# Optimization experiments

Hardware: AMD Instinct MI355X
Metric: run time of the kernel (lower is better)

Reference implementation:

```python
import jax, jax.numpy as jnp
import numpy as np

B, H, L, E = 32, 8, 512, 3
N_VARS = 8
TOP_P = 0.5
NOISE_EPS = 0.01
EPS = 1e-10


def setup_inputs() -> dict:
    key = jax.random.key(0)
    k1, k2, k3 = jax.random.split(key, 3)
    scale = 1.0 / np.sqrt(L)  # sane logits for softmax
    x = jax.random.normal(k1, (B, H, L, L), dtype=jnp.float32)
    gate_w = jax.random.normal(k2, (E, L), dtype=jnp.float32) * scale
    noise_w = jax.random.normal(k3, (E, L), dtype=jnp.float32) * scale
    return {"x": x, "gate_w": gate_w, "noise_w": noise_w}


def _build_masks(L, n_vars):
    # Vectorized version of the torch per-k loop building [L, 3, L] masks.
    N = L // n_vars
    j = jnp.arange(L)          # target position
    k = jnp.arange(L)[:, None]  # source position
    S = ((j % N == k % N) & (j != k)).astype(jnp.float32)   # same offset, different var
    T = ((j // N) == (k // N)).astype(jnp.float32)           # same variable block
    ST = 1.0 - S - T
    return jnp.stack([S, T, ST], axis=1)  # [L, 3, L]


def _noisy_top_p_gating(xf, gate_w, noise_w, key):
    # xf: [BH, L, L] -> logits [BH, L, E]
    clean_logits = jnp.einsum('ble,ne->bln', xf, gate_w)
    noise_stddev = jax.nn.softplus(jnp.einsum('ble,ne->bln', xf, noise_w)) + NOISE_EPS
    noisy_logits = clean_logits + jax.random.normal(key, clean_logits.shape, clean_logits.dtype) * noise_stddev
    probs = jax.nn.softmax(noisy_logits, axis=-1)  # softmax over experts (dim 2)
    # dynamic (entropy) loss: sum over L dim (dim=1), mean over rest
    loss_dynamic = -(probs * jnp.log(probs + EPS)).sum(axis=1).mean()
    # sort descending over experts
    order = jnp.argsort(-probs, axis=-1)
    sorted_probs = jnp.take_along_axis(probs, order, axis=-1)
    cum = jnp.cumsum(sorted_probs, axis=-1)
    mask = cum > TOP_P
    # keep the first expert that crosses the threshold
    thr_idx = jnp.argmax(mask.astype(jnp.int32), axis=-1)          # [BH, L]
    thr_mask = jnp.arange(E) == thr_idx[..., None]                 # one-hot bool
    mask = mask & ~thr_mask
    # scatter kept (mask==0) sorted positions back to original expert ids:
    # top_p_mask[..., sorted_indices[..., k]] = (mask[..., k] == 0)
    inv = jnp.argsort(order, axis=-1)
    top_p_mask = jnp.take_along_axis((~mask).astype(jnp.float32), inv, axis=-1)
    # importance loss on masked sorted probs summed over batch dim
    kept = jnp.where(mask, 0.0, sorted_probs)
    importance = kept.sum(axis=0)  # [L, E]
    loss_importance = jnp.var(importance, ddof=1) / (importance.mean() ** 2 + EPS)
    loss = loss_importance + 0.1 * loss_dynamic
    return top_p_mask, loss


def reference(x, gate_w, noise_w):
    Bx, Hx, Lx, _ = x.shape
    xf = x.reshape(Bx * Hx, Lx, Lx)
    gates, loss = _noisy_top_p_gating(xf, gate_w, noise_w, jax.random.key(42))
    gates = gates.reshape(Bx, Hx, Lx, E).astype(jnp.float32)
    masks = _build_masks(Lx, N_VARS)            # [L, 3, L]
    mask_base = jnp.eye(Lx, dtype=jnp.float32)[None, None]
    out = jnp.einsum('bhli,lid->bhld', gates, masks) + mask_base
    return (out, loss)
```

## Files before the change

### kernel.cpp

```cpp
#include <hip/hip_runtime.h>
#include <cstdint>
#include <cstddef>


namespace {

constexpr int kBH = 256;
constexpr int kL = 512;
constexpr int kE = 3;
constexpr int kRows = kBH * kL;

__device__ __forceinline__ uint32_t rotl32(uint32_t v, int n) {
  return (v << n) | (v >> (32 - n));
}

__device__ __forceinline__ void threefry2x32_k42(uint32_t& x0, uint32_t& x1) {
  const uint32_t ks0 = 0u;
  const uint32_t ks1 = 42u;
  const uint32_t ks2 = 0u ^ 42u ^ 0x1BD11BDAu;
  x0 += ks0; x1 += ks1;
#define TF_ROUND(r) { x0 += x1; x1 = rotl32(x1, (r)); x1 ^= x0; }
  TF_ROUND(13) TF_ROUND(15) TF_ROUND(26) TF_ROUND(6)
  x0 += ks1; x1 += ks2 + 1u;
  TF_ROUND(17) TF_ROUND(29) TF_ROUND(16) TF_ROUND(24)
  x0 += ks2; x1 += ks0 + 2u;
  TF_ROUND(13) TF_ROUND(15) TF_ROUND(26) TF_ROUND(6)
  x0 += ks0; x1 += ks1 + 3u;
  TF_ROUND(17) TF_ROUND(29) TF_ROUND(16) TF_ROUND(24)
  x0 += ks1; x1 += ks2 + 4u;
  TF_ROUND(13) TF_ROUND(15) TF_ROUND(26) TF_ROUND(6)
  x0 += ks2; x1 += ks0 + 5u;
#undef TF_ROUND
}

__device__ __forceinline__ uint32_t jax_random_bits(uint32_t flat_idx) {
  uint32_t x0 = 0u;
  uint32_t x1 = flat_idx;
  threefry2x32_k42(x0, x1);
  return x0 ^ x1;
}

__device__ float bits_to_normal(uint32_t bits) {
#pragma clang fp contract(off)
  const uint32_t fb = (bits >> 9) | 0x3F800000u;
  const float f = __uint_as_float(fb) - 1.0f;
  const float lo = -0.99999994f;
  float u = f * 2.0f + lo;
  u = fmaxf(lo, u);
  float w = -log1pf(-(u * u));
  float p;
  if (w < 5.0f) {
    w = w - 2.5f;
    p = 2.81022636e-08f;
    p = 3.43273939e-07f + p * w;
    p = -3.5233877e-06f + p * w;
    p = -4.39150654e-06f + p * w;
    p = 0.00021858087f + p * w;
    p = -0.00125372503f + p * w;
    p = -0.00417768164f + p * w;
    p = 0.246640727f + p * w;
    p = 1.50140941f + p * w;
  } else {
    w = sqrtf(w) - 3.0f;
    p = -0.000200214257f;
    p = 0.000100950558f + p * w;
    p = 0.00134934322f + p * w;
    p = -0.00367342844f + p * w;
    p = 0.00573950773f + p * w;
    p = -0.0076224613f + p * w;
    p = 0.00943887047f + p * w;
    p = 1.00167406f + p * w;
    p = 2.83297682f + p * w;
  }
  const float einv = p * u;
  return 1.41421354f * einv;
}

__device__ __forceinline__ float softplus_f32(float v) {
#pragma clang fp contract(off)
  const float amax = fmaxf(v, 0.0f);
  return amax + log1pf(expf(-fabsf(v)));
}

#define LOADG(BUF, OFF)                                                     \
  _Pragma("unroll")                                                         \
  for (int i_ = 0; i_ < 4; ++i_)                                            \
    BUF[i_] = *reinterpret_cast<const float4*>(xr + (OFF) + i_ * 4);

#define COMP16(BUF, KB)                                                     \
  {                                                                         \
    _Pragma("unroll")                                                       \
    for (int j_ = 0; j_ < 4; ++j_) {                                        \
      const int k_ = (KB) + j_ * 4;                                         \
      const float4 wg0 = *reinterpret_cast<const float4*>(gw + k_);         \
      const float4 wg1 = *reinterpret_cast<const float4*>(gw + kL + k_);    \
      const float4 wg2 = *reinterpret_cast<const float4*>(gw + 2*kL + k_);  \
      const float4 wn0 = *reinterpret_cast<const float4*>(nw + k_);         \
      const float4 wn1 = *reinterpret_cast<const float4*>(nw + kL + k_);    \
      const float4 wn2 = *reinterpret_cast<const float4*>(nw + 2*kL + k_);  \
      const float4 xq = BUF[j_];                                            \
      accg[0] = fmaf(xq.x, wg0.x, accg[0]);                                 \
      accg[1] = fmaf(xq.x, wg1.x, accg[1]);                                 \
      accg[2] = fmaf(xq.x, wg2.x, accg[2]);                                 \
      accn[0] = fmaf(xq.x, wn0.x, accn[0]);                                 \
      accn[1] = fmaf(xq.x, wn1.x, accn[1]);                                 \
      accn[2] = fmaf(xq.x, wn2.x, accn[2]);                                 \
      accg[0] = fmaf(xq.y, wg0.y, accg[0]);                                 \
      accg[1] = fmaf(xq.y, wg1.y, accg[1]);                                 \
      accg[2] = fmaf(xq.y, wg2.y, accg[2]);                                 \
      accn[0] = fmaf(xq.y, wn0.y, accn[0]);                                 \
      accn[1] = fmaf(xq.y, wn1.y, accn[1]);                                 \
      accn[2] = fmaf(xq.y, wn2.y, accn[2]);                                 \
      accg[0] = fmaf(xq.z, wg0.z, accg[0]);                                 \
      accg[1] = fmaf(xq.z, wg1.z, accg[1]);                                 \
      accg[2] = fmaf(xq.z, wg2.z, accg[2]);                                 \
      accn[0] = fmaf(xq.z, wn0.z, accn[0]);                                 \
      accn[1] = fmaf(xq.z, wn1.z, accn[1]);                                 \
      accn[2] = fmaf(xq.z, wn2.z, accn[2]);                                 \
      accg[0] = fmaf(xq.w, wg0.w, accg[0]);                                 \
      accg[1] = fmaf(xq.w, wg1.w, accg[1]);                                 \
      accg[2] = fmaf(xq.w, wg2.w, accg[2]);                                 \
      accn[0] = fmaf(xq.w, wn0.w, accn[0]);                                 \
      accn[1] = fmaf(xq.w, wn1.w, accn[1]);                                 \
      accn[2] = fmaf(xq.w, wn2.w, accn[2]);                                 \
    }                                                                       \
  }

__global__ __launch_bounds__(256) void gating_kernel(
    const float* __restrict__ x, const float* __restrict__ gw,
    const float* __restrict__ nw, float* __restrict__ g_out,
    float* __restrict__ kept_out, float* __restrict__ ent_out) {
  const int t = threadIdx.x;
  const int r = blockIdx.x * 256 + t;
  const float* xr = x + (size_t)r * kL;

  float accg[3] = {0.f, 0.f, 0.f};
  float accn[3] = {0.f, 0.f, 0.f};
  {
    float4 bufA[4], bufB[4];
    LOADG(bufA, 0)
    for (int k0 = 0; k0 < kL; k0 += 32) {
      LOADG(bufB, k0 + 16)
      COMP16(bufA, k0)
      if (k0 + 32 < kL) { LOADG(bufA, k0 + 32) }
      COMP16(bufB, k0 + 16)
    }
  }

  {
#pragma clang fp contract(off)
    float noisy[3];
    const uint32_t nbase = (uint32_t)r * 3u;
#pragma unroll
    for (int e = 0; e < 3; ++e) {
      const float cl = accg[e];
      const float sp = softplus_f32(accn[e]) + 0.01f;
      const float nz = bits_to_normal(jax_random_bits(nbase + (uint32_t)e));
      const float prod = nz * sp;
      noisy[e] = cl + prod;
    }
    const float m = fmaxf(noisy[0], fmaxf(noisy[1], noisy[2]));
    float uu[3];
    uu[0] = expf(noisy[0] - m);
    uu[1] = expf(noisy[1] - m);
    uu[2] = expf(noisy[2] - m);
    const float ssum = (uu[0] + uu[1]) + uu[2];
    float p[3];
    p[0] = uu[0] / ssum;
    p[1] = uu[1] / ssum;
    p[2] = uu[2] / ssum;

    int o0 = 0;
    if (p[1] > p[o0]) o0 = 1;
    if (p[2] > p[o0]) o0 = 2;
    const int i = (o0 == 0) ? 1 : 0;
    const int j = (o0 == 2) ? 1 : 2;
    const int o1 = (p[j] > p[i]) ? j : i;

    const float s0 = p[o0];
    const float s1 = p[o1];
    const bool keep2 = !(s0 > 0.5f);

    float g[3] = {0.f, 0.f, 0.f};
    g[o0] = 1.f;
    if (keep2) g[o1] = 1.f;

    float ent = 0.f;
    ent += p[0] * logf(p[0] + 1e-10f);
    ent += p[1] * logf(p[1] + 1e-10f);
    ent += p[2] * logf(p[2] + 1e-10f);

    const int bh = r >> 9;
    const int l = r & (kL - 1);
    g_out[r * 3 + 0] = g[0];
    g_out[r * 3 + 1] = g[1];
    g_out[r * 3 + 2] = g[2];
    kept_out[(0 * kL + l) * kBH + bh] = s0;
    kept_out[(1 * kL + l) * kBH + bh] = keep2 ? s1 : 0.f;
    kept_out[(2 * kL + l) * kBH + bh] = 0.f;
    ent_out[r] = -ent;
  }
}

__global__ __launch_bounds__(256) void loss_partial_kernel(
    const float* __restrict__ kept, const float* __restrict__ ent,
    double* __restrict__ imp_ws, double* __restrict__ ent_ws) {
  __shared__ double red[256];
  const int t = threadIdx.x;
  const int ln = t & 63;
  const int wg = blockIdx.x * 4 + (t >> 6);

#pragma unroll
  for (int rep = 0; rep < 3; ++rep) {
    const int q = wg + rep * 512;
    const float4 v = reinterpret_cast<const float4*>(kept + (size_t)q * kBH)[ln];
    double s = ((double)v.x + (double)v.y) + ((double)v.z + (double)v.w);
#pragma unroll
    for (int off = 32; off > 0; off >>= 1) s += __shfl_xor(s, off, 64);
    if (ln == 0) imp_ws[q] = s;
  }

  double a = 0.0;
#pragma unroll
  for (int it = 0; it < 4; ++it) {
    a += (double)ent[blockIdx.x * 1024 + it * 256 + t];
  }
  red[t] = a;
  __syncthreads();
  for (int off = 128; off > 0; off >>= 1) {
    if (t < off) red[t] += red[t + off];
    __syncthreads();
  }
  if (t == 0) ent_ws[blockIdx.x] = red[0];
}

__global__ __launch_bounds__(256) void loss_final_kernel(
    const double* __restrict__ imp_ws, const double* __restrict__ ent_ws,
    float* __restrict__ loss_out) {
  __shared__ double red[256];
  __shared__ double s_mean;
  const int t = threadIdx.x;

  double a = 0.0;
  for (int i = t; i < kL * kE; i += 256) a += imp_ws[i];
  red[t] = a;
  __syncthreads();
  for (int off = 128; off > 0; off >>= 1) {
    if (t < off) red[t] += red[t + off];
    __syncthreads();
  }
  if (t == 0) s_mean = red[0] / (double)(kL * kE);
  __syncthreads();
  const double mean = s_mean;

  double sq = 0.0;
  for (int i = t; i < kL * kE; i += 256) {
    const double d = imp_ws[i] - mean;
    sq += d * d;
  }
  red[t] = sq;
  __syncthreads();
  for (int off = 128; off > 0; off >>= 1) {
    if (t < off) red[t] += red[t + off];
    __syncthreads();
  }
  const double var_sum = red[0];
  __syncthreads();

  double e = 0.0;
  for (int i = t; i < 128; i += 256) e += ent_ws[i];
  red[t] = e;
  __syncthreads();
  for (int off = 128; off > 0; off >>= 1) {
    if (t < off) red[t] += red[t + off];
    __syncthreads();
  }
  if (t == 0) {
    const double var = var_sum / (double)(kL * kE - 1);
    const double loss_imp = var / (mean * mean + 1e-10);
    const double loss_dyn = red[0] / 768.0;
    loss_out[0] = (float)(loss_imp + 0.1 * loss_dyn);
  }
}

__global__ __launch_bounds__(256) void out_kernel(
    const float* __restrict__ g, float* __restrict__ out) {
  const int td = threadIdx.x;
  const int r = blockIdx.x * 8 + (td >> 5);
  const int l = r & (kL - 1);
  const float g0 = g[r * 3 + 0];
  const float g1 = g[r * 3 + 1];
  const float g2 = g[r * 3 + 2];
  const int lblk = l >> 6;
  const int loff = l & 63;
  float* orow = out + (size_t)r * kL;
  const int c0 = (td & 31) * 4;
#pragma unroll
  for (int j = 0; j < 4; ++j) {
    const int d0 = c0 + j * 128;
    float vals[4];
#pragma unroll
    for (int k = 0; k < 4; ++k) {
      const int d = d0 + k;
      float v;
      if (((d & 63) == loff) && (d != l)) v = g0;
      else if ((d >> 6) == lblk) v = g1;
      else v = g2;
      if (d == l) v += 1.0f;
      vals[k] = v;
    }
    *reinterpret_cast<float4*>(orow + d0) = *reinterpret_cast<float4*>(vals);
  }
}

}

extern "C" void kernel_launch(void* const* d_in, const int* in_sizes, int n_in,
                              void* d_out, int out_size, void* d_ws, size_t ws_size,
                              hipStream_t stream) {
  (void)in_sizes; (void)n_in; (void)out_size; (void)ws_size;
  const float* x = (const float*)d_in[0];
  const float* gw = (const float*)d_in[1];
  const float* nw = (const float*)d_in[2];
  float* out = (float*)d_out;

  float* ws = (float*)d_ws;
  float* ws_g = ws;
  float* ws_kept = ws + (size_t)kRows * 3;
  float* ws_ent = ws + (size_t)kRows * 6;
  double* ws_imp = (double*)(ws + (size_t)kRows * 7);
  double* ws_entp = ws_imp + kL * kE;

  gating_kernel<<<kRows / 256, 256, 0, stream>>>(x, gw, nw, ws_g, ws_kept, ws_ent);
  loss_partial_kernel<<<128, 256, 0, stream>>>(ws_kept, ws_ent, ws_imp, ws_entp);
  loss_final_kernel<<<1, 256, 0, stream>>>(ws_imp, ws_entp,
                                           out + (size_t)kBH * kL * kL);
  out_kernel<<<kRows / 8, 256, 0, stream>>>(ws_g, out);
}
```

Before: 142.2 us.

## Split gating dot products across six threads per row with separate epilogue kernel

The fused gating kernel gave each thread a full row and six dot products. It is now split into two kernels. A dot kernel assigns six threads to each row, one per weight vector, and writes the six accumulators to workspace. A new epilogue kernel reads them back and does the noise, softmax and top-p logic. This raises thread-level parallelism and shortens each thread's dependency chain, at the cost of an extra launch, an extra workspace round trip, and each row of x being read by six threads. Those reads hit the same cache lines but are uncoalesced across the row.

```diff
diff --git a/kernel.cpp b/kernel.cpp
--- a/kernel.cpp
+++ b/kernel.cpp
@@ -82,70 +82,54 @@
   return amax + log1pf(expf(-fabsf(v)));
 }
 
-#define LOADG(BUF, OFF)                                                     \
+#define LD4(B, P, OFF)                                                      \
   _Pragma("unroll")                                                         \
   for (int i_ = 0; i_ < 4; ++i_)                                            \
-    BUF[i_] = *reinterpret_cast<const float4*>(xr + (OFF) + i_ * 4);
-
-#define COMP16(BUF, KB)                                                     \
+    B[i_] = *reinterpret_cast<const float4*>((P) + (OFF) + i_ * 4);
+
+#define CH16(XB, WB)                                                        \
   {                                                                         \
     _Pragma("unroll")                                                       \
     for (int j_ = 0; j_ < 4; ++j_) {                                        \
-      const int k_ = (KB) + j_ * 4;                                         \
-      const float4 wg0 = *reinterpret_cast<const float4*>(gw + k_);         \
-      const float4 wg1 = *reinterpret_cast<const float4*>(gw + kL + k_);    \
-      const float4 wg2 = *reinterpret_cast<const float4*>(gw + 2*kL + k_);  \
-      const float4 wn0 = *reinterpret_cast<const float4*>(nw + k_);         \
-      const float4 wn1 = *reinterpret_cast<const float4*>(nw + kL + k_);    \
-      const float4 wn2 = *reinterpret_cast<const float4*>(nw + 2*kL + k_);  \
-      const float4 xq = BUF[j_];                                            \
-      accg[0] = fmaf(xq.x, wg0.x, accg[0]);                                 \
-      accg[1] = fmaf(xq.x, wg1.x, accg[1]);                                 \
-      accg[2] = fmaf(xq.x, wg2.x, accg[2]);                                 \
-      accn[0] = fmaf(xq.x, wn0.x, accn[0]);                                 \
-      accn[1] = fmaf(xq.x, wn1.x, accn[1]);                                 \
-      accn[2] = fmaf(xq.x, wn2.x, accn[2]);                                 \
-      accg[0] = fmaf(xq.y, wg0.y, accg[0]);                                 \
-      accg[1] = fmaf(xq.y, wg1.y, accg[1]);                                 \
-      accg[2] = fmaf(xq.y, wg2.y, accg[2]);                                 \
-      accn[0] = fmaf(xq.y, wn0.y, accn[0]);                                 \
-      accn[1] = fmaf(xq.y, wn1.y, accn[1]);                                 \
-      accn[2] = fmaf(xq.y, wn2.y, accn[2]);                                 \
-      accg[0] = fmaf(xq.z, wg0.z, accg[0]);                                 \
-      accg[1] = fmaf(xq.z, wg1.z, accg[1]);                                 \
-      accg[2] = fmaf(xq.z, wg2.z, accg[2]);                                 \
-      accn[0] = fmaf(xq.z, wn0.z, accn[0]);                                 \
-      accn[1] = fmaf(xq.z, wn1.z, accn[1]);                                 \
-      accn[2] = fmaf(xq.z, wn2.z, accn[2]);                                 \
-      accg[0] = fmaf(xq.w, wg0.w, accg[0]);                                 \
-      accg[1] = fmaf(xq.w, wg1.w, accg[1]);                                 \
-      accg[2] = fmaf(xq.w, wg2.w, accg[2]);                                 \
-      accn[0] = fmaf(xq.w, wn0.w, accn[0]);                                 \
-      accn[1] = fmaf(xq.w, wn1.w, accn[1]);                                 \
-      accn[2] = fmaf(xq.w, wn2.w, accn[2]);                                 \
+      acc = fmaf(XB[j_].x, WB[j_].x, acc);                                  \
+      acc = fmaf(XB[j_].y, WB[j_].y, acc);                                  \
+      acc = fmaf(XB[j_].z, WB[j_].z, acc);                                  \
+      acc = fmaf(XB[j_].w, WB[j_].w, acc);                                  \
     }                                                                       \
   }
 
-__global__ __launch_bounds__(256) void gating_kernel(
+__global__ __launch_bounds__(192) void dot_kernel(
     const float* __restrict__ x, const float* __restrict__ gw,
-    const float* __restrict__ nw, float* __restrict__ g_out,
+    const float* __restrict__ nw, float* __restrict__ acc_out) {
+  const int t = threadIdx.x;
+  const int row_ib = t / 6;
+  const int chain = t - row_ib * 6;
+  const int r = blockIdx.x * 32 + row_ib;
+  const float* xr = x + (size_t)r * kL;
+  const float* wr = (chain < 3) ? (gw + chain * kL) : (nw + (chain - 3) * kL);
+
+  float acc = 0.f;
+  {
+#pragma clang fp contract(off)
+    float4 xA[4], xB[4], wA[4], wB[4];
+    LD4(xA, xr, 0) LD4(wA, wr, 0)
+    for (int k0 = 0; k0 < kL; k0 += 32) {
+      LD4(xB, xr, k0 + 16) LD4(wB, wr, k0 + 16)
+      CH16(xA, wA)
+      if (k0 + 32 < kL) { LD4(xA, xr, k0 + 32) LD4(wA, wr, k0 + 32) }
+      CH16(xB, wB)
+    }
+  }
+  acc_out[(size_t)blockIdx.x * 192 + t] = acc;
+}
+
+__global__ __launch_bounds__(256) void epilogue_kernel(
+    const float* __restrict__ acc_in, float* __restrict__ g_out,
     float* __restrict__ kept_out, float* __restrict__ ent_out) {
-  const int t = threadIdx.x;
-  const int r = blockIdx.x * 256 + t;
-  const float* xr = x + (size_t)r * kL;
-
-  float accg[3] = {0.f, 0.f, 0.f};
-  float accn[3] = {0.f, 0.f, 0.f};
-  {
-    float4 bufA[4], bufB[4];
-    LOADG(bufA, 0)
-    for (int k0 = 0; k0 < kL; k0 += 32) {
-      LOADG(bufB, k0 + 16)
-      COMP16(bufA, k0)
-      if (k0 + 32 < kL) { LOADG(bufA, k0 + 32) }
-      COMP16(bufB, k0 + 16)
-    }
-  }
+  const int r = blockIdx.x * 256 + threadIdx.x;
+  const float* a = acc_in + (size_t)r * 6;
+  float accg[3] = {a[0], a[1], a[2]};
+  float accn[3] = {a[3], a[4], a[5]};
 
   {
 #pragma clang fp contract(off)
@@ -328,10 +312,12 @@
   float* ws_g = ws;
   float* ws_kept = ws + (size_t)kRows * 3;
   float* ws_ent = ws + (size_t)kRows * 6;
-  double* ws_imp = (double*)(ws + (size_t)kRows * 7);
+  float* ws_acc = ws + (size_t)kRows * 7;
+  double* ws_imp = (double*)(ws + (size_t)kRows * 13 + (size_t)kRows);
   double* ws_entp = ws_imp + kL * kE;
 
-  gating_kernel<<<kRows / 256, 256, 0, stream>>>(x, gw, nw, ws_g, ws_kept, ws_ent);
+  dot_kernel<<<kRows / 32, 192, 0, stream>>>(x, gw, nw, ws_acc);
+  epilogue_kernel<<<kRows / 256, 256, 0, stream>>>(ws_acc, ws_g, ws_kept, ws_ent);
   loss_partial_kernel<<<128, 256, 0, stream>>>(ws_kept, ws_ent, ws_imp, ws_entp);
   loss_final_kernel<<<1, 256, 0, stream>>>(ws_imp, ws_entp,
                                            out + (size_t)kBH * kL * kL);
```

After: 293.8 us. 2.07x slower.
